# Performance work log

Hardware: AMD Instinct MI355X
Metric: run time of the kernel (lower is better)

The kernel has to match this reference:

```python
import math
import jax, jax.numpy as jnp
import numpy as np

H = 512        # d_model
NST = 32       # N // 2 complex states
M = 2          # frac_M
CH = 1         # channels
L_DEFAULT = 2048
OMIN, OMAX = 1e-06, 100.0
EMIN, EMAX = 1e-06, 10.0


def _logit_init(vals, vmin, vmax):
    v = np.clip(np.asarray(vals, np.float32), vmin, vmax)
    p = np.clip((v - vmin) / (vmax - vmin), 1e-06, 1.0 - 1e-06)
    return np.log(p / (1.0 - p)).astype(np.float32)


def setup_inputs() -> dict:
    key = jax.random.key(0)
    k1, k2 = jax.random.split(key, 2)
    # log_dt ~ U[log(dt_min), log(dt_max)]
    log_dt = (jax.random.uniform(k1, (H,), dtype=jnp.float32)
              * (math.log(0.1) - math.log(0.001)) + math.log(0.001))
    # C stored as real view of complex [CH, H, NST]
    C_real = jax.random.normal(k2, (CH, H, NST, 2), dtype=jnp.float32)
    log_A_real = jnp.log(0.5 * jnp.ones((H, NST), jnp.float32))
    A_imag = math.pi * jnp.broadcast_to(jnp.arange(NST, dtype=jnp.float32), (H, NST))
    # frac_M == 2 defaults: omega=[0.0, 0.1], eta=[1.0, 0.1], stored as logits
    omega_logit = jnp.asarray(_logit_init([0.0, 0.1], OMIN, OMAX))
    eta_logit = jnp.asarray(_logit_init([1.0, 0.1], EMIN, EMAX))
    return {"C_real": C_real, "log_dt": log_dt, "log_A_real": log_A_real,
            "A_imag": A_imag, "omega_logit": omega_logit,
            "eta_logit": eta_logit, "L": L_DEFAULT}


def reference(C_real, log_dt, log_A_real, A_imag, omega_logit, eta_logit, L):
    dt = jnp.exp(log_dt)                                   # [H]
    C = C_real[..., 0] + 1j * C_real[..., 1]               # [CH, H, NST] complex
    A = -jnp.exp(log_A_real) + 1j * A_imag                 # [H, NST] complex
    omega = OMIN + jax.nn.sigmoid(omega_logit) * (OMAX - OMIN)  # [M]
    eta = EMIN + jax.nn.sigmoid(eta_logit) * (EMAX - EMIN)      # [M]
    # fractional mixture of poles: A_frac[h, m, n] = -omega_m + eta_m * A[h, n]
    A_frac = (-omega[None, :, None] + eta[None, :, None] * A[:, None, :]).reshape(H, M * NST)
    C_frac = (eta[None, None, :, None] * C[:, :, None, :]).reshape(CH, H, M * NST)
    dtA = A_frac * dt[:, None]                             # [H, M*NST]
    exp_dtA = jnp.exp(dtA)
    small = jnp.abs(A_frac) < 1e-06
    C_disc = C_frac * (exp_dtA[None] - 1.0) / (A_frac[None] + 1e-08)
    C_disc = jnp.where(small[None], C_frac * dt[None, :, None], C_disc)
    t = jnp.arange(L, dtype=jnp.float32)
    exp_K = jnp.exp(dtA[:, :, None] * t)                   # [H, M*NST, L] complex Vandermonde
    K = 2.0 * jnp.einsum('chn,hnl->chl', C_disc, exp_K).real  # [CH, H, L]
    return K
```

## Files before the change

kernel.cpp:

```cpp
#include <hip/hip_runtime.h>
#include <math.h>

#define HH   512
#define NST  32
#define MM   2
#define LL   2048
#define NS   (MM * NST)
#define TL   8

__global__ __launch_bounds__(256) void loong_kernel(
    const float* __restrict__ C_real,
    const float* __restrict__ log_dt,
    const float* __restrict__ log_A_real,
    const float* __restrict__ A_imag,
    const float* __restrict__ omega_logit,
    const float* __restrict__ eta_logit,
    float* __restrict__ out)
{
    __shared__ float sCdr[NS], sCdi[NS], swr[NS], swi[NS], sar[NS], sai[NS];
    const int h = blockIdx.x;
    const int t = threadIdx.x;

    if (t < NS) {
        const int m = t >> 5;
        const int n = t & 31;
        const float dt  = __expf(log_dt[h]);
        const float Are = -__expf(log_A_real[h * NST + n]);
        const float Aim = A_imag[h * NST + n];
        const float om = 1e-6f + (100.0f - 1e-6f) * (1.0f / (1.0f + __expf(-omega_logit[m])));
        const float et = 1e-6f + (10.0f  - 1e-6f) * (1.0f / (1.0f + __expf(-eta_logit[m])));
        const float Afr = fmaf(et, Are, -om);
        const float Afi = et * Aim;
        const float Cfr = et * C_real[(h * NST + n) * 2 + 0];
        const float Cfi = et * C_real[(h * NST + n) * 2 + 1];
        const float ar = dt * Afr, ai = dt * Afi;
        const float e  = __expf(ar);
        float sn, cs;
        __sincosf(ai, &sn, &cs);
        const float Er = e * cs, Ei = e * sn;
        const float dr = Afr + 1e-8f, di = Afi;
        const float inv = 1.0f / fmaf(dr, dr, di * di);
        const float numr = Er - 1.0f, numi = Ei;
        const float qr = fmaf(numr, dr,  numi * di) * inv;
        const float qi = fmaf(numi, dr, -numr * di) * inv;
        float Cdr = fmaf(Cfr, qr, -(Cfi * qi));
        float Cdi = fmaf(Cfr, qi,  (Cfi * qr));
        if (sqrtf(fmaf(Afr, Afr, Afi * Afi)) < 1e-6f) {
            Cdr = Cfr * dt;
            Cdi = Cfi * dt;
        }
        sCdr[t] = 2.0f * Cdr;
        sCdi[t] = 2.0f * Cdi;
        swr[t] = Er;  swi[t] = Ei;
        sar[t] = ar;  sai[t] = ai;
    }
    __syncthreads();

    float acc[TL];
#pragma unroll
    for (int j = 0; j < TL; ++j) acc[j] = 0.0f;

    const float l0 = (float)(t * TL);

    for (int s = 0; s < NS; s += 2) {
        const float ar0 = sar[s],     ai0 = sai[s];
        const float ar1 = sar[s + 1], ai1 = sai[s + 1];
        const float e0 = __expf(ar0 * l0);
        const float e1 = __expf(ar1 * l0);
        float s0, c0, s1, c1;
        __sincosf(ai0 * l0, &s0, &c0);
        __sincosf(ai1 * l0, &s1, &c1);
        float zr0 = e0 * c0, zi0 = e0 * s0;
        float zr1 = e1 * c1, zi1 = e1 * s1;
        const float wr0 = swr[s],     wi0 = swi[s];
        const float wr1 = swr[s + 1], wi1 = swi[s + 1];
        const float Cr0 = sCdr[s],     Ci0 = sCdi[s];
        const float Cr1 = sCdr[s + 1], Ci1 = sCdi[s + 1];
#pragma unroll
        for (int j = 0; j < TL; ++j) {
            acc[j] = fmaf(Cr0, zr0, acc[j]);
            acc[j] = fmaf(-Ci0, zi0, acc[j]);
            acc[j] = fmaf(Cr1, zr1, acc[j]);
            acc[j] = fmaf(-Ci1, zi1, acc[j]);
            const float nzr0 = fmaf(zr0, wr0, -(zi0 * wi0));
            const float nzi0 = fmaf(zr0, wi0,  (zi0 * wr0));
            const float nzr1 = fmaf(zr1, wr1, -(zi1 * wi1));
            const float nzi1 = fmaf(zr1, wi1,  (zi1 * wr1));
            zr0 = nzr0; zi0 = nzi0;
            zr1 = nzr1; zi1 = nzi1;
        }
    }

    float4* o = reinterpret_cast<float4*>(out + (size_t)h * LL + (size_t)t * TL);
    o[0] = make_float4(acc[0], acc[1], acc[2], acc[3]);
    o[1] = make_float4(acc[4], acc[5], acc[6], acc[7]);
}

extern "C" void kernel_launch(void* const* d_in, const int* in_sizes, int n_in,
                              void* d_out, int out_size, void* d_ws, size_t ws_size,
                              hipStream_t stream) {
    const float* C_real      = (const float*)d_in[0];
    const float* log_dt      = (const float*)d_in[1];
    const float* log_A_real  = (const float*)d_in[2];
    const float* A_imag      = (const float*)d_in[3];
    const float* omega_logit = (const float*)d_in[4];
    const float* eta_logit   = (const float*)d_in[5];
    float* out = (float*)d_out;

    loong_kernel<<<dim3(HH), dim3(256), 0, stream>>>(
        C_real, log_dt, log_A_real, A_imag, omega_logit, eta_logit, out);
}
```

Measured before the change: 80.64 us.

## Split sequence across two blocks per channel and fold C into the recurrence

Each channel's 2048 outputs are now split across two blocks, so 1024 blocks are launched with 4 outputs per thread instead of 8. C is premultiplied into the starting Vandermonde term, so the inner loop only adds the real part and advances the complex rotation. States are handled in groups of four. Shared memory is packed into float4/float2, and the phase is range-reduced with floor before sincos to keep the fast intrinsic accurate. The cost is that the per-channel discretisation setup now runs twice, and each thread evaluates exp/sincos for every state over only 4 outputs, so there is more transcendental work per output.

Result: faster. 78.93 us (-2.1%).

```diff
diff --git a/kernel.cpp b/kernel.cpp
--- a/kernel.cpp
+++ b/kernel.cpp
@@ -1,12 +1,17 @@
 #include <hip/hip_runtime.h>
 #include <math.h>
 
-#define HH   512
-#define NST  32
-#define MM   2
-#define LL   2048
-#define NS   (MM * NST)
-#define TL   8
+#define HH      512
+#define NST     32
+#define MM      2
+#define LL      2048
+#define NS      (MM * NST)
+#define TL      4
+#define NCHUNK  2
+#define CHUNK_L (256 * TL)
+
+#define TWO_PI     6.2831853071795864f
+#define INV_TWO_PI 0.15915494309189535f
 
 __global__ __launch_bounds__(256) void loong_kernel(
     const float* __restrict__ C_real,
@@ -17,9 +22,13 @@
     const float* __restrict__ eta_logit,
     float* __restrict__ out)
 {
-    __shared__ float sCdr[NS], sCdi[NS], swr[NS], swi[NS], sar[NS], sai[NS];
-    const int h = blockIdx.x;
-    const int t = threadIdx.x;
+    __shared__ float4 sP[NS];
+    __shared__ float2 sA[NS];
+
+    const int bid   = blockIdx.x;
+    const int h     = bid >> 1;
+    const int chunk = bid & 1;
+    const int t     = threadIdx.x;
 
     if (t < NS) {
         const int m = t >> 5;
@@ -49,10 +58,8 @@
             Cdr = Cfr * dt;
             Cdi = Cfi * dt;
         }
-        sCdr[t] = 2.0f * Cdr;
-        sCdi[t] = 2.0f * Cdi;
-        swr[t] = Er;  swi[t] = Ei;
-        sar[t] = ar;  sai[t] = ai;
+        sP[t] = make_float4(2.0f * Cdr, 2.0f * Cdi, Er, Ei);
+        sA[t] = make_float2(ar, ai * INV_TWO_PI);
     }
     __syncthreads();
 
@@ -60,40 +67,41 @@
 #pragma unroll
     for (int j = 0; j < TL; ++j) acc[j] = 0.0f;
 
-    const float l0 = (float)(t * TL);
+    const float l0 = (float)(chunk * CHUNK_L + t * TL);
 
-    for (int s = 0; s < NS; s += 2) {
-        const float ar0 = sar[s],     ai0 = sai[s];
-        const float ar1 = sar[s + 1], ai1 = sai[s + 1];
-        const float e0 = __expf(ar0 * l0);
-        const float e1 = __expf(ar1 * l0);
-        float s0, c0, s1, c1;
-        __sincosf(ai0 * l0, &s0, &c0);
-        __sincosf(ai1 * l0, &s1, &c1);
-        float zr0 = e0 * c0, zi0 = e0 * s0;
-        float zr1 = e1 * c1, zi1 = e1 * s1;
-        const float wr0 = swr[s],     wi0 = swi[s];
-        const float wr1 = swr[s + 1], wi1 = swi[s + 1];
-        const float Cr0 = sCdr[s],     Ci0 = sCdi[s];
-        const float Cr1 = sCdr[s + 1], Ci1 = sCdi[s + 1];
+    for (int s = 0; s < NS; s += 4) {
+        float yr[4], yi[4], wr[4], wi[4];
+#pragma unroll
+        for (int u = 0; u < 4; ++u) {
+            const float4 P = sP[s + u];
+            const float2 A = sA[s + u];
+            const float e = __expf(A.x * l0);
+            float p = A.y * l0;
+            p = p - floorf(p);
+            float sn, cs;
+            __sincosf(p * TWO_PI, &sn, &cs);
+            const float zr = e * cs, zi = e * sn;
+            yr[u] = fmaf(P.x, zr, -(P.y * zi));
+            yi[u] = fmaf(P.x, zi,  (P.y * zr));
+            wr[u] = P.z; wi[u] = P.w;
+        }
 #pragma unroll
         for (int j = 0; j < TL; ++j) {
-            acc[j] = fmaf(Cr0, zr0, acc[j]);
-            acc[j] = fmaf(-Ci0, zi0, acc[j]);
-            acc[j] = fmaf(Cr1, zr1, acc[j]);
-            acc[j] = fmaf(-Ci1, zi1, acc[j]);
-            const float nzr0 = fmaf(zr0, wr0, -(zi0 * wi0));
-            const float nzi0 = fmaf(zr0, wi0,  (zi0 * wr0));
-            const float nzr1 = fmaf(zr1, wr1, -(zi1 * wi1));
-            const float nzi1 = fmaf(zr1, wi1,  (zi1 * wr1));
-            zr0 = nzr0; zi0 = nzi0;
-            zr1 = nzr1; zi1 = nzi1;
+#pragma unroll
+            for (int u = 0; u < 4; ++u) {
+                acc[j] += yr[u];
+                if (j + 1 < TL) {
+                    const float nr = fmaf(yr[u], wr[u], -(yi[u] * wi[u]));
+                    const float ni = fmaf(yr[u], wi[u],  (yi[u] * wr[u]));
+                    yr[u] = nr; yi[u] = ni;
+                }
+            }
         }
     }
 
-    float4* o = reinterpret_cast<float4*>(out + (size_t)h * LL + (size_t)t * TL);
+    float4* o = reinterpret_cast<float4*>(
+        out + (size_t)h * LL + (size_t)(chunk * CHUNK_L) + (size_t)t * TL);
     o[0] = make_float4(acc[0], acc[1], acc[2], acc[3]);
-    o[1] = make_float4(acc[4], acc[5], acc[6], acc[7]);
 }
 
 extern "C" void kernel_launch(void* const* d_in, const int* in_sizes, int n_in,
@@ -107,6 +115,6 @@
     const float* eta_logit   = (const float*)d_in[5];
     float* out = (float*)d_out;
 
-    loong_kernel<<<dim3(HH), dim3(256), 0, stream>>>(
+    loong_kernel<<<dim3(HH * NCHUNK), dim3(256), 0, stream>>>(
         C_real, log_dt, log_A_real, A_imag, omega_logit, eta_logit, out);
 }
```

## Replace per-thread exp/sincos with factored power tables and real two-term recurrence

Applied to the files above, without the earlier changes.

Each block now precomputes two shared-memory tables per pole: low powers w^(8r) with w^(8r+1), and high powers C*w^(128q) together with the recurrence coefficients 2Re(w) and -|w|^2. Every thread builds its starting value from one product of a low and a high entry, then advances the real part with a scalar two-term recurrence instead of a complex multiply per step. This removes the transcendental calls and most complex multiplies from the hot loop. The costs are more serial setup work for 64 threads, larger shared-memory traffic, and possible accuracy drift from the repeated squaring and the recurrence.

Result: faster. 73.98 us (-8.3%).

```diff
diff --git a/kernel.cpp b/kernel.cpp
--- a/kernel.cpp
+++ b/kernel.cpp
@@ -17,81 +17,107 @@
     const float* __restrict__ eta_logit,
     float* __restrict__ out)
 {
-    __shared__ float sCdr[NS], sCdi[NS], swr[NS], swi[NS], sar[NS], sai[NS];
-    const int h = blockIdx.x;
-    const int t = threadIdx.x;
+    __shared__ float4 sT1[NS][16];
+    __shared__ float4 sT2[NS][16];
 
-    if (t < NS) {
-        const int m = t >> 5;
-        const int n = t & 31;
-        const float dt  = __expf(log_dt[h]);
-        const float Are = -__expf(log_A_real[h * NST + n]);
+    const int h   = blockIdx.x;
+    const int tid = threadIdx.x;
+
+    if (tid < NS) {
+        const int m = tid >> 5;
+        const int n = tid & 31;
+        const float dt  = expf(log_dt[h]);
+        const float Are = -expf(log_A_real[h * NST + n]);
         const float Aim = A_imag[h * NST + n];
-        const float om = 1e-6f + (100.0f - 1e-6f) * (1.0f / (1.0f + __expf(-omega_logit[m])));
-        const float et = 1e-6f + (10.0f  - 1e-6f) * (1.0f / (1.0f + __expf(-eta_logit[m])));
+        const float om = 1e-6f + (100.0f - 1e-6f) / (1.0f + expf(-omega_logit[m]));
+        const float et = 1e-6f + (10.0f  - 1e-6f) / (1.0f + expf(-eta_logit[m]));
         const float Afr = fmaf(et, Are, -om);
         const float Afi = et * Aim;
         const float Cfr = et * C_real[(h * NST + n) * 2 + 0];
         const float Cfi = et * C_real[(h * NST + n) * 2 + 1];
         const float ar = dt * Afr, ai = dt * Afi;
-        const float e  = __expf(ar);
+        const float e = expf(ar);
         float sn, cs;
-        __sincosf(ai, &sn, &cs);
+        sincosf(ai, &sn, &cs);
         const float Er = e * cs, Ei = e * sn;
         const float dr = Afr + 1e-8f, di = Afi;
         const float inv = 1.0f / fmaf(dr, dr, di * di);
         const float numr = Er - 1.0f, numi = Ei;
-        const float qr = fmaf(numr, dr,  numi * di) * inv;
-        const float qi = fmaf(numi, dr, -numr * di) * inv;
-        float Cdr = fmaf(Cfr, qr, -(Cfi * qi));
-        float Cdi = fmaf(Cfr, qi,  (Cfi * qr));
+        const float fr = fmaf(numr, dr,  numi * di) * inv;
+        const float fi = fmaf(numi, dr, -numr * di) * inv;
+        float Cdr = fmaf(Cfr, fr, -(Cfi * fi));
+        float Cdi = fmaf(Cfr, fi,  (Cfi * fr));
         if (sqrtf(fmaf(Afr, Afr, Afi * Afi)) < 1e-6f) {
             Cdr = Cfr * dt;
             Cdi = Cfi * dt;
         }
-        sCdr[t] = 2.0f * Cdr;
-        sCdi[t] = 2.0f * Cdi;
-        swr[t] = Er;  swi[t] = Ei;
-        sar[t] = ar;  sai[t] = ai;
+        const float Ccr = 2.0f * Cdr, Cci = 2.0f * Cdi;
+        const float p  = 2.0f * Er;
+        const float qc = -fmaf(Er, Er, Ei * Ei);
+
+        float w2r = fmaf(Er, Er, -(Ei * Ei)),  w2i = 2.0f * Er * Ei;
+        float w4r = fmaf(w2r, w2r, -(w2i * w2i)), w4i = 2.0f * w2r * w2i;
+        float w8r = fmaf(w4r, w4r, -(w4i * w4i)), w8i = 2.0f * w4r * w4i;
+
+        float ur = 1.0f, ui = 0.0f;
+#pragma unroll
+        for (int r = 0; r < 16; ++r) {
+            sT1[tid][r] = make_float4(ur, ui,
+                                      fmaf(ur, Er, -(ui * Ei)),
+                                      fmaf(ur, Ei,  (ui * Er)));
+            const float nr = fmaf(ur, w8r, -(ui * w8i));
+            const float ni = fmaf(ur, w8i,  (ui * w8r));
+            ur = nr; ui = ni;
+        }
+        float wr_ = w8r, wi_ = w8i;
+#pragma unroll
+        for (int k = 0; k < 4; ++k) {
+            const float nr = fmaf(wr_, wr_, -(wi_ * wi_));
+            const float ni = 2.0f * wr_ * wi_;
+            wr_ = nr; wi_ = ni;
+        }
+        float vr = Ccr, vi = Cci;
+#pragma unroll
+        for (int q = 0; q < 16; ++q) {
+            sT2[tid][q] = make_float4(vr, vi, p, qc);
+            const float nr = fmaf(vr, wr_, -(vi * wi_));
+            const float ni = fmaf(vr, wi_,  (vi * wr_));
+            vr = nr; vi = ni;
+        }
     }
     __syncthreads();
+
+    const int ri = tid & 15;
+    const int qi = tid >> 4;
 
     float acc[TL];
 #pragma unroll
     for (int j = 0; j < TL; ++j) acc[j] = 0.0f;
 
-    const float l0 = (float)(t * TL);
-
-    for (int s = 0; s < NS; s += 2) {
-        const float ar0 = sar[s],     ai0 = sai[s];
-        const float ar1 = sar[s + 1], ai1 = sai[s + 1];
-        const float e0 = __expf(ar0 * l0);
-        const float e1 = __expf(ar1 * l0);
-        float s0, c0, s1, c1;
-        __sincosf(ai0 * l0, &s0, &c0);
-        __sincosf(ai1 * l0, &s1, &c1);
-        float zr0 = e0 * c0, zi0 = e0 * s0;
-        float zr1 = e1 * c1, zi1 = e1 * s1;
-        const float wr0 = swr[s],     wi0 = swi[s];
-        const float wr1 = swr[s + 1], wi1 = swi[s + 1];
-        const float Cr0 = sCdr[s],     Ci0 = sCdi[s];
-        const float Cr1 = sCdr[s + 1], Ci1 = sCdi[s + 1];
+    for (int s = 0; s < NS; s += 4) {
+        float4 t1[4], t2[4];
 #pragma unroll
-        for (int j = 0; j < TL; ++j) {
-            acc[j] = fmaf(Cr0, zr0, acc[j]);
-            acc[j] = fmaf(-Ci0, zi0, acc[j]);
-            acc[j] = fmaf(Cr1, zr1, acc[j]);
-            acc[j] = fmaf(-Ci1, zi1, acc[j]);
-            const float nzr0 = fmaf(zr0, wr0, -(zi0 * wi0));
-            const float nzi0 = fmaf(zr0, wi0,  (zi0 * wr0));
-            const float nzr1 = fmaf(zr1, wr1, -(zi1 * wi1));
-            const float nzi1 = fmaf(zr1, wi1,  (zi1 * wr1));
-            zr0 = nzr0; zi0 = nzi0;
-            zr1 = nzr1; zi1 = nzi1;
+        for (int u = 0; u < 4; ++u) {
+            t1[u] = sT1[s + u][ri];
+            t2[u] = sT2[s + u][qi];
+        }
+#pragma unroll
+        for (int u = 0; u < 4; ++u) {
+            const float p = t2[u].z, qq = t2[u].w;
+            float r0 = fmaf(t1[u].x, t2[u].x, -(t1[u].y * t2[u].y));
+            float r1 = fmaf(t1[u].z, t2[u].x, -(t1[u].w * t2[u].y));
+            acc[0] += r0;
+            acc[1] += r1;
+#pragma unroll
+            for (int j = 2; j < TL; ++j) {
+                const float rn = fmaf(p, r1, qq * r0);
+                acc[j] += rn;
+                r0 = r1; r1 = rn;
+            }
         }
     }
 
-    float4* o = reinterpret_cast<float4*>(out + (size_t)h * LL + (size_t)t * TL);
+    float4* o = reinterpret_cast<float4*>(out + (size_t)h * LL + (size_t)tid * TL);
     o[0] = make_float4(acc[0], acc[1], acc[2], acc[3]);
     o[1] = make_float4(acc[4], acc[5], acc[6], acc[7]);
 }
```
